# Optimization experiments

Hardware: AMD Instinct MI355X
Metric: run time of the kernel (lower is better)

## Reference

```python
import jax, jax.numpy as jnp
import numpy as np

VOCAB = 32000
DIM = 768
DEPTH = 4
D_STATE = 16
D_CONV = 4
EXPAND = 2
D_INNER = DIM * EXPAND          # 1536
DT_RANK = -(-DIM // 16)         # ceil(768/16) = 48
BATCH, SEQ = 2, 2048
EPS = 1e-5


def setup_inputs() -> dict:
    key = jax.random.key(0)
    ks = jax.random.split(key, 16)
    s = 0.02
    inp = {
        "input_ids": jax.random.randint(ks[0], (BATCH, SEQ), 0, VOCAB, dtype=jnp.int64) if jax.config.read('jax_enable_x64') else jax.random.randint(ks[0], (BATCH, SEQ), 0, VOCAB, dtype=jnp.int32),
        "emb": s * jax.random.normal(ks[1], (VOCAB, DIM), jnp.float32),
        "W_in": s * jax.random.normal(ks[2], (DEPTH, 2 * D_INNER, DIM), jnp.float32),
        "conv_w": s * jax.random.normal(ks[3], (DEPTH, D_INNER, D_CONV), jnp.float32),
        "conv_b": s * jax.random.normal(ks[4], (DEPTH, D_INNER), jnp.float32),
        "W_x": s * jax.random.normal(ks[5], (DEPTH, DT_RANK + 2 * D_STATE, D_INNER), jnp.float32),
        "W_dt": s * jax.random.normal(ks[6], (DEPTH, D_INNER, DT_RANK), jnp.float32),
        "b_dt": jnp.zeros((DEPTH, D_INNER), jnp.float32),
        "A_log": jnp.tile(jnp.log(jnp.arange(1, D_STATE + 1, dtype=jnp.float32))[None, None, :], (DEPTH, D_INNER, 1)),
        "Dp": jnp.ones((DEPTH, D_INNER), jnp.float32),
        "W_out": s * jax.random.normal(ks[7], (DEPTH, DIM, D_INNER), jnp.float32),
        "ln_g": jnp.ones((DIM,), jnp.float32),
        "ln_b": jnp.zeros((DIM,), jnp.float32),
        "W_head": s * jax.random.normal(ks[8], (VOCAB, DIM), jnp.float32),
    }
    return inp


def _mamba_block(x, W_in, conv_w, conv_b, W_x, W_dt, b_dt, A_log, Dp, W_out):
    # x: [B, L, dim]
    B_, L, _ = x.shape
    xz = x @ W_in.T                               # [B, L, 2*D_INNER]
    x_in, z = jnp.split(xz, 2, axis=-1)
    # causal depthwise conv1d (torch padding=d_conv-1 then truncate to L)
    x_pad = jnp.pad(x_in, ((0, 0), (D_CONV - 1, 0), (0, 0)))
    x_conv = conv_b + sum(x_pad[:, k:k + L, :] * conv_w[:, k] for k in range(D_CONV))
    x_ssm = jax.nn.silu(x_conv)                   # [B, L, D_INNER]
    dbl = x_ssm @ W_x.T                           # [B, L, DT_RANK + 2*D_STATE]
    dt = jax.nn.softplus(dbl[..., :DT_RANK] @ W_dt.T + b_dt)  # [B, L, D_INNER]
    Bm = dbl[..., DT_RANK:DT_RANK + D_STATE]      # [B, L, D_STATE]
    Cm = dbl[..., DT_RANK + D_STATE:]             # [B, L, D_STATE]
    A = -jnp.exp(A_log)                           # [D_INNER, D_STATE]

    def step(h, inp):
        dt_t, x_t, B_t, C_t = inp                 # [B,Din],[B,Din],[B,ds],[B,ds]
        dA = jnp.exp(dt_t[:, :, None] * A)
        h = h * dA + (dt_t * x_t)[:, :, None] * B_t[:, None, :]
        y_t = jnp.einsum('bds,bs->bd', h, C_t)
        return h, y_t

    h0 = jnp.zeros((B_, D_INNER, D_STATE), x.dtype)
    xs = (dt.transpose(1, 0, 2), x_ssm.transpose(1, 0, 2),
          Bm.transpose(1, 0, 2), Cm.transpose(1, 0, 2))
    _, ys = jax.lax.scan(step, h0, xs)            # [L, B, D_INNER]
    y = ys.transpose(1, 0, 2) + x_ssm * Dp
    return (y * jax.nn.silu(z)) @ W_out.T


def reference(input_ids, emb, W_in, conv_w, conv_b, W_x, W_dt, b_dt, A_log, Dp, W_out, ln_g, ln_b, W_head):
    x = emb[input_ids]                            # [B, L, dim]
    for i in range(DEPTH):                        # NOTE: no residual, as in source
        x = _mamba_block(x, W_in[i], conv_w[i], conv_b[i], W_x[i], W_dt[i],
                         b_dt[i], A_log[i], Dp[i], W_out[i])
    mu = jnp.mean(x, axis=-1, keepdims=True)
    var = jnp.mean(jnp.square(x - mu), axis=-1, keepdims=True)
    x = (x - mu) * jax.lax.rsqrt(var + EPS) * ln_g + ln_b
    logits = x @ W_head.T                         # [B, L, VOCAB]
    return logits
```

## Files before the change

### kernel.cpp

```cpp
#include <hip/hip_runtime.h>
#include <hip/hip_bf16.h>

#define DMODEL 768
#define DINNER 1536
#define NROWS  4096
#define SEQLEN 2048
#define DSTATE 16
#define DTRANK 48
#define DXP    80
#define NVOCAB 32000
#define TCHUNK 64
#define NCHUNK 32

typedef unsigned short u16;
typedef __attribute__((ext_vector_type(8))) short  short8;
typedef __attribute__((ext_vector_type(4))) float  floatx4;

__device__ __forceinline__ u16 f2bf(float f) {
    unsigned u = __builtin_bit_cast(unsigned, f);
    unsigned r = 0x7FFFu + ((u >> 16) & 1u);
    return (u16)((u + r) >> 16);
}
__device__ __forceinline__ float bf2f(u16 h) {
    unsigned u = ((unsigned)h) << 16;
    return __builtin_bit_cast(float, u);
}
__device__ __forceinline__ float siluf(float x) { return x / (1.f + expf(-x)); }
__device__ __forceinline__ float softplusf(float x) {
    return fmaxf(x, 0.f) + log1pf(__expf(-fabsf(x)));
}

__global__ void k_split(const float* __restrict__ in, u16* __restrict__ hi,
                        u16* __restrict__ lo, int n4) {
    int i = blockIdx.x * blockDim.x + threadIdx.x;
    int stride = gridDim.x * blockDim.x;
    for (; i < n4; i += stride) {
        float4 f = ((const float4*)in)[i];
        u16 h0 = f2bf(f.x), h1 = f2bf(f.y), h2 = f2bf(f.z), h3 = f2bf(f.w);
        ushort4 hv; hv.x = h0; hv.y = h1; hv.z = h2; hv.w = h3;
        ((ushort4*)hi)[i] = hv;
        if (lo) {
            ushort4 lv;
            lv.x = f2bf(f.x - bf2f(h0));
            lv.y = f2bf(f.y - bf2f(h1));
            lv.z = f2bf(f.z - bf2f(h2));
            lv.w = f2bf(f.w - bf2f(h3));
            ((ushort4*)lo)[i] = lv;
        }
    }
}

__global__ void k_embed(const int* __restrict__ ids, const float* __restrict__ emb,
                        float* __restrict__ x) {
    int row = blockIdx.x;
    int id = ids[row];
    const float* src = emb + (size_t)id * DMODEL;
    float* dst = x + (size_t)row * DMODEL;
    for (int c = threadIdx.x; c < DMODEL; c += blockDim.x) dst[c] = src[c];
}

__global__ void k_conv_silu(const float* __restrict__ xz, const float* __restrict__ cw,
                            const float* __restrict__ cb, float* __restrict__ ssm,
                            float* __restrict__ sz) {
    int row = blockIdx.y;
    int d   = blockIdx.x * blockDim.x + threadIdx.x;
    int t   = row & (SEQLEN - 1);
    float acc = cb[d];
    #pragma unroll
    for (int k = 0; k < 4; ++k) {
        int tt = t + k - 3;
        if (tt >= 0) acc += xz[(size_t)(row + k - 3) * (2 * DINNER) + d] * cw[d * 4 + k];
    }
    ssm[(size_t)row * DINNER + d] = siluf(acc);
    float z = xz[(size_t)row * (2 * DINNER) + DINNER + d];
    sz[(size_t)row * DINNER + d] = siluf(z);
}

__global__ void k_softplus(float* __restrict__ dtp, const float* __restrict__ bd, int n4) {
    int i = blockIdx.x * blockDim.x + threadIdx.x;
    int stride = gridDim.x * blockDim.x;
    for (; i < n4; i += stride) {
        float4 v = ((float4*)dtp)[i];
        int d = (i * 4) % DINNER;
        float4 b = *(const float4*)&bd[d];
        v.x = softplusf(v.x + b.x);
        v.y = softplusf(v.y + b.y);
        v.z = softplusf(v.z + b.z);
        v.w = softplusf(v.w + b.w);
        ((float4*)dtp)[i] = v;
    }
}

__global__ void k_scan1(const float* __restrict__ dtp, const float* __restrict__ ssm,
                        const float* __restrict__ dbl, const float* __restrict__ Alog,
                        float* __restrict__ hend, float* __restrict__ Pout) {
    int ch   = blockIdx.x;
    int b    = blockIdx.y / (DINNER / 16);
    int dblk = blockIdx.y % (DINNER / 16);
    int dl = threadIdx.x >> 4;
    int s  = threadIdx.x & 15;
    int d  = dblk * 16 + dl;
    float A = -__expf(Alog[d * DSTATE + s]);
    float h = 0.f, P = 1.f;
    size_t row = (size_t)b * SEQLEN + (size_t)ch * TCHUNK;
    for (int t = 0; t < TCHUNK; ++t, ++row) {
        float dt = dtp[row * DINNER + d];
        float xv = ssm[row * DINNER + d];
        float Bv = dbl[row * DXP + DTRANK + s];
        float dA = __expf(dt * A);
        h = h * dA + dt * xv * Bv;
        P *= dA;
    }
    size_t o = (((size_t)b * NCHUNK + ch) * DINNER + d) * DSTATE + s;
    hend[o] = h;
    Pout[o] = P;
}

__global__ void k_scan2(const float* __restrict__ hend, const float* __restrict__ P,
                        float* __restrict__ h0) {
    int idx = blockIdx.x * blockDim.x + threadIdx.x;
    int b  = idx / (DINNER * DSTATE);
    int ds = idx % (DINNER * DSTATE);
    float h = 0.f;
    size_t base = (size_t)b * NCHUNK * DINNER * DSTATE + ds;
    for (int c = 0; c < NCHUNK; ++c) {
        size_t o = base + (size_t)c * (DINNER * DSTATE);
        h0[o] = h;
        h = hend[o] + P[o] * h;
    }
}

__global__ void k_scan3(const float* __restrict__ dtp, const float* __restrict__ ssm,
                        const float* __restrict__ dbl, const float* __restrict__ Alog,
                        const float* __restrict__ Dpv, const float* __restrict__ sz,
                        const float* __restrict__ h0, float* __restrict__ u) {
    int ch   = blockIdx.x;
    int b    = blockIdx.y / (DINNER / 16);
    int dblk = blockIdx.y % (DINNER / 16);
    int dl = threadIdx.x >> 4;
    int s  = threadIdx.x & 15;
    int d  = dblk * 16 + dl;
    float A  = -__expf(Alog[d * DSTATE + s]);
    float Dd = Dpv[d];
    float h  = h0[(((size_t)b * NCHUNK + ch) * DINNER + d) * DSTATE + s];
    size_t row = (size_t)b * SEQLEN + (size_t)ch * TCHUNK;
    for (int t = 0; t < TCHUNK; ++t, ++row) {
        float dt = dtp[row * DINNER + d];
        float xv = ssm[row * DINNER + d];
        float Bv = dbl[row * DXP + DTRANK + s];
        float Cv = dbl[row * DXP + DTRANK + DSTATE + s];
        float dA = __expf(dt * A);
        h = h * dA + dt * xv * Bv;
        float yv = h * Cv;
        yv += __shfl_xor(yv, 1);
        yv += __shfl_xor(yv, 2);
        yv += __shfl_xor(yv, 4);
        yv += __shfl_xor(yv, 8);
        if (s == 0) u[row * DINNER + d] = (yv + xv * Dd) * sz[row * DINNER + d];
    }
}

__global__ void k_ln(const float* __restrict__ x, const float* __restrict__ g,
                     const float* __restrict__ bb, u16* __restrict__ out) {
    __shared__ float red[256];
    int row = blockIdx.x;
    int tid = threadIdx.x;
    const float* xr = x + (size_t)row * DMODEL;
    float v0 = xr[tid], v1 = xr[tid + 256], v2 = xr[tid + 512];
    red[tid] = v0 + v1 + v2;
    __syncthreads();
    for (int o = 128; o > 0; o >>= 1) { if (tid < o) red[tid] += red[tid + o]; __syncthreads(); }
    float mu = red[0] * (1.f / 768.f);
    __syncthreads();
    red[tid] = (v0 - mu) * (v0 - mu) + (v1 - mu) * (v1 - mu) + (v2 - mu) * (v2 - mu);
    __syncthreads();
    for (int o = 128; o > 0; o >>= 1) { if (tid < o) red[tid] += red[tid + o]; __syncthreads(); }
    float var = red[0] * (1.f / 768.f);
    float rs = rsqrtf(var + 1e-5f);
    u16* orow = out + (size_t)row * DMODEL;
    orow[tid]       = f2bf((v0 - mu) * rs * g[tid]       + bb[tid]);
    orow[tid + 256] = f2bf((v1 - mu) * rs * g[tid + 256] + bb[tid + 256]);
    orow[tid + 512] = f2bf((v2 - mu) * rs * g[tid + 512] + bb[tid + 512]);
}

template<int SPLIT>
__global__ __launch_bounds__(256, 2)
void k_gemm(const u16* __restrict__ Ah, const u16* __restrict__ Al,
            const u16* __restrict__ Bh, const u16* __restrict__ Bl,
            float* __restrict__ C, int M, int N, int K, int lda, int ldb, int ldc) {
    constexpr int LDK = 40;
    __shared__ __align__(16) u16 sA[2][128 * LDK];
    __shared__ __align__(16) u16 sB[2][128 * LDK];
    const int tid  = threadIdx.x;
    const int m0 = blockIdx.y * 128, n0 = blockIdx.x * 128;
    const int wave = tid >> 6, lane = tid & 63;
    const int wm = (wave >> 1) * 64, wn = (wave & 1) * 64;
    const int fr = lane & 15, fq = lane >> 4;

    floatx4 acc[4][4];
    #pragma unroll
    for (int i = 0; i < 4; ++i)
        #pragma unroll
        for (int j = 0; j < 4; ++j)
            #pragma unroll
            for (int r = 0; r < 4; ++r) acc[i][j][r] = 0.f;

    for (int kt = 0; kt < K; kt += 32) {
        __syncthreads();
        #pragma unroll
        for (int half = 0; half < 2; ++half) {
            int c  = tid + half * 256;
            int rr = c >> 2;
            int ko = (c & 3) * 8;
            int gk = kt + ko;
            {
                int gm = m0 + rr;
                short8 vh = {0,0,0,0,0,0,0,0}, vl = {0,0,0,0,0,0,0,0};
                if (gm < M) {
                    const u16* p = Ah + (size_t)gm * lda + gk;
                    if (gk + 8 <= K) vh = *(const short8*)p;
                    else { for (int jj = 0; jj < 8; ++jj) if (gk + jj < K) vh[jj] = (short)p[jj]; }
                    if (SPLIT) {
                        const u16* q = Al + (size_t)gm * lda + gk;
                        if (gk + 8 <= K) vl = *(const short8*)q;
                        else { for (int jj = 0; jj < 8; ++jj) if (gk + jj < K) vl[jj] = (short)q[jj]; }
                    }
                }
                *(short8*)&sA[0][rr * LDK + ko] = vh;
                if (SPLIT) *(short8*)&sA[1][rr * LDK + ko] = vl;
            }
            {
                int gn = n0 + rr;
                short8 vh = {0,0,0,0,0,0,0,0}, vl = {0,0,0,0,0,0,0,0};
                if (gn < N) {
                    const u16* p = Bh + (size_t)gn * ldb + gk;
                    if (gk + 8 <= K) vh = *(const short8*)p;
                    else { for (int jj = 0; jj < 8; ++jj) if (gk + jj < K) vh[jj] = (short)p[jj]; }
                    if (SPLIT) {
                        const u16* q = Bl + (size_t)gn * ldb + gk;
                        if (gk + 8 <= K) vl = *(const short8*)q;
                        else { for (int jj = 0; jj < 8; ++jj) if (gk + jj < K) vl[jj] = (short)q[jj]; }
                    }
                }
                *(short8*)&sB[0][rr * LDK + ko] = vh;
                if (SPLIT) *(short8*)&sB[1][rr * LDK + ko] = vl;
            }
        }
        __syncthreads();

        short8 aH[4], bH[4];
        #pragma unroll
        for (int i = 0; i < 4; ++i) aH[i] = *(const short8*)&sA[0][(wm + i * 16 + fr) * LDK + fq * 8];
        #pragma unroll
        for (int j = 0; j < 4; ++j) bH[j] = *(const short8*)&sB[0][(wn + j * 16 + fr) * LDK + fq * 8];
        #pragma unroll
        for (int i = 0; i < 4; ++i)
            #pragma unroll
            for (int j = 0; j < 4; ++j)
                acc[i][j] = __builtin_amdgcn_mfma_f32_16x16x32_bf16(aH[i], bH[j], acc[i][j], 0, 0, 0);
        if (SPLIT) {
            short8 aL[4], bL[4];
            #pragma unroll
            for (int i = 0; i < 4; ++i) aL[i] = *(const short8*)&sA[1][(wm + i * 16 + fr) * LDK + fq * 8];
            #pragma unroll
            for (int j = 0; j < 4; ++j) bL[j] = *(const short8*)&sB[1][(wn + j * 16 + fr) * LDK + fq * 8];
            #pragma unroll
            for (int i = 0; i < 4; ++i)
                #pragma unroll
                for (int j = 0; j < 4; ++j) {
                    acc[i][j] = __builtin_amdgcn_mfma_f32_16x16x32_bf16(aL[i], bH[j], acc[i][j], 0, 0, 0);
                    acc[i][j] = __builtin_amdgcn_mfma_f32_16x16x32_bf16(aH[i], bL[j], acc[i][j], 0, 0, 0);
                }
        }
    }
    #pragma unroll
    for (int i = 0; i < 4; ++i)
        #pragma unroll
        for (int j = 0; j < 4; ++j) {
            int m = m0 + wm + i * 16 + fq * 4;
            int n = n0 + wn + j * 16 + fr;
            if (n < N) {
                #pragma unroll
                for (int r = 0; r < 4; ++r)
                    if (m + r < M) C[(size_t)(m + r) * ldc + n] = acc[i][j][r];
            }
        }
}

extern "C" void kernel_launch(void* const* d_in, const int* in_sizes, int n_in,
                              void* d_out, int out_size, void* d_ws, size_t ws_size,
                              hipStream_t stream) {
    const int*   ids   = (const int*)d_in[0];
    const float* emb   = (const float*)d_in[1];
    const float* W_in  = (const float*)d_in[2];
    const float* cw    = (const float*)d_in[3];
    const float* cb    = (const float*)d_in[4];
    const float* W_x   = (const float*)d_in[5];
    const float* W_dt  = (const float*)d_in[6];
    const float* b_dt  = (const float*)d_in[7];
    const float* Alog  = (const float*)d_in[8];
    const float* Dp    = (const float*)d_in[9];
    const float* W_out = (const float*)d_in[10];
    const float* ln_g  = (const float*)d_in[11];
    const float* ln_b  = (const float*)d_in[12];
    const float* W_hd  = (const float*)d_in[13];

    char* ws = (char*)d_ws;
    float* xb   = (float*)(ws + 0);
    float* xz   = (float*)(ws + 12582912);
    float* ssm  = (float*)(ws + 62914560);
    float* szb  = (float*)(ws + 88080384);
    float* dbl  = (float*)(ws + 113246208);
    u16*   Ahb  = (u16*)(ws + 114556928);
    u16*   Alb  = (u16*)(ws + 127139840);
    u16*   Bhb  = (u16*)(ws + 139722752);
    u16*   Blb  = (u16*)(ws + 144441344);
    u16*   dblh = (u16*)(ws + 149159936);
    u16*   dbll = (u16*)(ws + 149815296);

    float* dtp = xz;
    float* ub  = xz + (size_t)NROWS * DINNER;
    u16*   lnh = Ahb;
    u16*   hdh = (u16*)xz;

    float* hendb = (float*)Ahb;
    float* Pb    = (float*)Alb;
    float* h0b   = (float*)Bhb;

    k_embed<<<NROWS, 256, 0, stream>>>(ids, emb, xb);

    for (int i = 0; i < 4; ++i) {
        k_split<<<2048, 256, 0, stream>>>(xb, Ahb, Alb, NROWS * DMODEL / 4);
        k_split<<<2048, 256, 0, stream>>>(W_in + (size_t)i * 3072 * DMODEL, Bhb, Blb, 3072 * DMODEL / 4);
        k_gemm<1><<<dim3(24, 32), 256, 0, stream>>>(Ahb, Alb, Bhb, Blb, xz,
                                                    NROWS, 3072, DMODEL, DMODEL, DMODEL, 3072);
        k_conv_silu<<<dim3(6, NROWS), 256, 0, stream>>>(xz, cw + (size_t)i * DINNER * 4,
                                                        cb + (size_t)i * DINNER, ssm, szb);
        k_split<<<2048, 256, 0, stream>>>(ssm, Ahb, Alb, NROWS * DINNER / 4);
        k_split<<<480, 256, 0, stream>>>(W_x + (size_t)i * DXP * DINNER, Bhb, Blb, DXP * DINNER / 4);
        k_gemm<1><<<dim3(1, 32), 256, 0, stream>>>(Ahb, Alb, Bhb, Blb, dbl,
                                                   NROWS, DXP, DINNER, DINNER, DINNER, DXP);
        k_split<<<320, 256, 0, stream>>>(dbl, dblh, dbll, NROWS * DXP / 4);
        k_split<<<72, 256, 0, stream>>>(W_dt + (size_t)i * DINNER * DTRANK, Bhb, Blb, DINNER * DTRANK / 4);
        k_gemm<1><<<dim3(12, 32), 256, 0, stream>>>(dblh, dbll, Bhb, Blb, dtp,
                                                    NROWS, DINNER, DTRANK, DXP, DTRANK, DINNER);
        k_softplus<<<2048, 256, 0, stream>>>(dtp, b_dt + (size_t)i * DINNER, NROWS * DINNER / 4);
        k_scan1<<<dim3(NCHUNK, 2 * (DINNER / 16)), 256, 0, stream>>>(
            dtp, ssm, dbl, Alog + (size_t)i * DINNER * DSTATE, hendb, Pb);
        k_scan2<<<192, 256, 0, stream>>>(hendb, Pb, h0b);
        k_scan3<<<dim3(NCHUNK, 2 * (DINNER / 16)), 256, 0, stream>>>(
            dtp, ssm, dbl, Alog + (size_t)i * DINNER * DSTATE,
            Dp + (size_t)i * DINNER, szb, h0b, ub);
        k_split<<<2048, 256, 0, stream>>>(ub, Ahb, Alb, NROWS * DINNER / 4);
        k_split<<<2048, 256, 0, stream>>>(W_out + (size_t)i * DMODEL * DINNER, Bhb, Blb, DMODEL * DINNER / 4);
        k_gemm<1><<<dim3(6, 32), 256, 0, stream>>>(Ahb, Alb, Bhb, Blb, xb,
                                                   NROWS, DMODEL, DINNER, DINNER, DINNER, DMODEL);
    }

    k_ln<<<NROWS, 256, 0, stream>>>(xb, ln_g, ln_b, lnh);
    k_split<<<8192, 256, 0, stream>>>(W_hd, hdh, (u16*)nullptr, NVOCAB * DMODEL / 4);
    k_gemm<0><<<dim3(250, 32), 256, 0, stream>>>(lnh, nullptr, hdh, nullptr, (float*)d_out,
                                                 NROWS, NVOCAB, DMODEL, DMODEL, DMODEL, NVOCAB);
}
```

Measured before the change: 3.095 ms.

## Add GEMM using direct global-to-LDS loads, XOR swizzle and XCD-aware tile mapping

Adds k_gemm_fast, a 128x128 bf16 MFMA GEMM that stages tiles with global_load_lds (direct global-to-LDS, bypassing registers). It stores them with an XOR swizzle to avoid LDS bank conflicts and remaps workgroup IDs so neighbouring tiles land on the same XCD for L2 reuse. It drops bounds checks and sets launch_bounds for 2 blocks per CU. It replaces the in_proj, out_proj and LM-head GEMMs and targets load latency and register pressure in the GEMM mainloop, at the cost of assuming all dimensions are tile multiples.

Measured after the change: 2.915 ms. -5.8%, faster.

```diff
diff --git a/kernel.cpp b/kernel.cpp
--- a/kernel.cpp
+++ b/kernel.cpp
@@ -28,6 +28,10 @@
 __device__ __forceinline__ float siluf(float x) { return x / (1.f + expf(-x)); }
 __device__ __forceinline__ float softplusf(float x) {
     return fmaxf(x, 0.f) + log1pf(__expf(-fabsf(x)));
+}
+__device__ __forceinline__ void gload_lds16(const u16* g, u16* l) {
+    __builtin_amdgcn_global_load_lds((const __attribute__((address_space(1))) void*)g,
+                                     (__attribute__((address_space(3))) void*)l, 16, 0, 0);
 }
 
 __global__ void k_split(const float* __restrict__ in, u16* __restrict__ hi,
@@ -287,6 +291,94 @@
         }
 }
 
+template<int SPLIT>
+__global__ __launch_bounds__(256, 2)
+void k_gemm_fast(const u16* __restrict__ Ah, const u16* __restrict__ Al,
+                 const u16* __restrict__ Bh, const u16* __restrict__ Bl,
+                 float* __restrict__ C, int lda, int ldb, int ldc, int K) {
+    __shared__ __align__(16) u16 sA[SPLIT + 1][128 * 32];
+    __shared__ __align__(16) u16 sB[SPLIT + 1][128 * 32];
+    const int nx = gridDim.x;
+    const int nwg = nx * gridDim.y;
+    const int lin = blockIdx.y * nx + blockIdx.x;
+    const int qq = nwg >> 3, rr8 = nwg & 7;
+    const int xcd = lin & 7, jj = lin >> 3;
+    const int swz = (xcd < rr8 ? xcd * (qq + 1) : rr8 * (qq + 1) + (xcd - rr8) * qq) + jj;
+    const int n0 = (swz % nx) * 128, m0 = (swz / nx) * 128;
+
+    const int tid  = threadIdx.x;
+    const int wave = tid >> 6, lane = tid & 63;
+    const int wm = (wave >> 1) * 64, wn = (wave & 1) * 64;
+    const int fr = lane & 15, fq = lane >> 4;
+
+    const int srow = (wave << 5) + (lane >> 2);
+    const int scol = (((lane & 3) ^ ((lane >> 2) & 3)) << 3);
+    const int ldsoff0 = (wave << 5) * 32;
+
+    floatx4 acc[4][4];
+    #pragma unroll
+    for (int i = 0; i < 4; ++i)
+        #pragma unroll
+        for (int j = 0; j < 4; ++j)
+            #pragma unroll
+            for (int r = 0; r < 4; ++r) acc[i][j][r] = 0.f;
+
+    for (int kt = 0; kt < K; kt += 32) {
+        __syncthreads();
+        #pragma unroll
+        for (int qi = 0; qi < 2; ++qi) {
+            const int row = srow + qi * 16;
+            const int lo  = ldsoff0 + (qi << 4) * 32;
+            gload_lds16(Ah + (size_t)(m0 + row) * lda + kt + scol, &sA[0][lo]);
+            gload_lds16(Bh + (size_t)(n0 + row) * ldb + kt + scol, &sB[0][lo]);
+            if constexpr (SPLIT) {
+                gload_lds16(Al + (size_t)(m0 + row) * lda + kt + scol, &sA[1][lo]);
+                gload_lds16(Bl + (size_t)(n0 + row) * ldb + kt + scol, &sB[1][lo]);
+            }
+        }
+        __syncthreads();
+
+        short8 aH[4], bH[4];
+        #pragma unroll
+        for (int i = 0; i < 4; ++i)
+            aH[i] = *(const short8*)&sA[0][(wm + i * 16 + fr) * 32 + ((fq ^ (fr & 3)) << 3)];
+        #pragma unroll
+        for (int j = 0; j < 4; ++j)
+            bH[j] = *(const short8*)&sB[0][(wn + j * 16 + fr) * 32 + ((fq ^ (fr & 3)) << 3)];
+        #pragma unroll
+        for (int i = 0; i < 4; ++i)
+            #pragma unroll
+            for (int j = 0; j < 4; ++j)
+                acc[i][j] = __builtin_amdgcn_mfma_f32_16x16x32_bf16(aH[i], bH[j], acc[i][j], 0, 0, 0);
+        if constexpr (SPLIT) {
+            short8 aL[4], bL[4];
+            #pragma unroll
+            for (int i = 0; i < 4; ++i)
+                aL[i] = *(const short8*)&sA[1][(wm + i * 16 + fr) * 32 + ((fq ^ (fr & 3)) << 3)];
+            #pragma unroll
+            for (int j = 0; j < 4; ++j)
+                bL[j] = *(const short8*)&sB[1][(wn + j * 16 + fr) * 32 + ((fq ^ (fr & 3)) << 3)];
+            #pragma unroll
+            for (int i = 0; i < 4; ++i)
+                #pragma unroll
+                for (int j = 0; j < 4; ++j) {
+                    acc[i][j] = __builtin_amdgcn_mfma_f32_16x16x32_bf16(aL[i], bH[j], acc[i][j], 0, 0, 0);
+                    acc[i][j] = __builtin_amdgcn_mfma_f32_16x16x32_bf16(aH[i], bL[j], acc[i][j], 0, 0, 0);
+                }
+        }
+    }
+    #pragma unroll
+    for (int i = 0; i < 4; ++i)
+        #pragma unroll
+        for (int j = 0; j < 4; ++j) {
+            int m = m0 + wm + i * 16 + fq * 4;
+            int n = n0 + wn + j * 16 + fr;
+            #pragma unroll
+            for (int r = 0; r < 4; ++r)
+                C[(size_t)(m + r) * ldc + n] = acc[i][j][r];
+        }
+}
+
 extern "C" void kernel_launch(void* const* d_in, const int* in_sizes, int n_in,
                               void* d_out, int out_size, void* d_ws, size_t ws_size,
                               hipStream_t stream) {
@@ -332,8 +424,8 @@
     for (int i = 0; i < 4; ++i) {
         k_split<<<2048, 256, 0, stream>>>(xb, Ahb, Alb, NROWS * DMODEL / 4);
         k_split<<<2048, 256, 0, stream>>>(W_in + (size_t)i * 3072 * DMODEL, Bhb, Blb, 3072 * DMODEL / 4);
-        k_gemm<1><<<dim3(24, 32), 256, 0, stream>>>(Ahb, Alb, Bhb, Blb, xz,
-                                                    NROWS, 3072, DMODEL, DMODEL, DMODEL, 3072);
+        k_gemm_fast<1><<<dim3(24, 32), 256, 0, stream>>>(Ahb, Alb, Bhb, Blb, xz,
+                                                         DMODEL, DMODEL, 3072, DMODEL);
         k_conv_silu<<<dim3(6, NROWS), 256, 0, stream>>>(xz, cw + (size_t)i * DINNER * 4,
                                                         cb + (size_t)i * DINNER, ssm, szb);
         k_split<<<2048, 256, 0, stream>>>(ssm, Ahb, Alb, NROWS * DINNER / 4);
@@ -353,12 +445,12 @@
             Dp + (size_t)i * DINNER, szb, h0b, ub);
         k_split<<<2048, 256, 0, stream>>>(ub, Ahb, Alb, NROWS * DINNER / 4);
         k_split<<<2048, 256, 0, stream>>>(W_out + (size_t)i * DMODEL * DINNER, Bhb, Blb, DMODEL * DINNER / 4);
-        k_gemm<1><<<dim3(6, 32), 256, 0, stream>>>(Ahb, Alb, Bhb, Blb, xb,
-                                                   NROWS, DMODEL, DINNER, DINNER, DINNER, DMODEL);
+        k_gemm_fast<1><<<dim3(6, 32), 256, 0, stream>>>(Ahb, Alb, Bhb, Blb, xb,
+                                                        DINNER, DINNER, DMODEL, DINNER);
     }
 
     k_ln<<<NROWS, 256, 0, stream>>>(xb, ln_g, ln_b, lnh);
     k_split<<<8192, 256, 0, stream>>>(W_hd, hdh, (u16*)nullptr, NVOCAB * DMODEL / 4);
-    k_gemm<0><<<dim3(250, 32), 256, 0, stream>>>(lnh, nullptr, hdh, nullptr, (float*)d_out,
-                                                 NROWS, NVOCAB, DMODEL, DMODEL, DMODEL, NVOCAB);
-}
+    k_gemm_fast<0><<<dim3(250, 32), 256, 0, stream>>>(lnh, nullptr, hdh, nullptr, (float*)d_out,
+                                                      DMODEL, DMODEL, NVOCAB, DMODEL);
+}
```
